# Performance work log

Hardware: AMD Instinct MI355X
Metric: run time of the kernel (lower is better)

Reference implementation:

```python
import jax, jax.numpy as jnp
import numpy as np

INPUT_DIM = 256
DEPTH = 8
HIDDEN = 64
NUM_INNER = 2 ** DEPTH - 1   # 255
NUM_LEAVES = 2 ** DEPTH      # 256
BATCH = 8192


def _xavier(key, shape, fan_in, fan_out):
    bound = jnp.sqrt(6.0 / (fan_in + fan_out)).astype(jnp.float32)
    return jax.random.uniform(key, shape, jnp.float32, -bound, bound)


def setup_inputs() -> dict:
    key = jax.random.key(0)
    k = jax.random.split(key, 5)
    x = jax.random.normal(k[0], (BATCH, INPUT_DIM), jnp.float32)
    # Batched per-node MLP params (one slice per inner node)
    w1 = _xavier(k[1], (NUM_INNER, HIDDEN, INPUT_DIM), INPUT_DIM, HIDDEN)
    b1 = jnp.zeros((NUM_INNER, HIDDEN), jnp.float32)
    w2 = _xavier(k[2], (NUM_INNER, HIDDEN), HIDDEN, 1)
    b2 = jnp.zeros((NUM_INNER,), jnp.float32)
    leaf = _xavier(k[3], (NUM_LEAVES, 1), NUM_LEAVES, 1)
    return {"x": x, "w1": w1, "b1": b1, "w2": w2, "b2": b2, "leaf": leaf}


def reference(x, w1, b1, w2, b2, leaf):
    B = x.shape[0]
    # Fused per-node MLPs: hidden [B, N, H]
    h = jax.nn.relu(jnp.einsum("bi,nhi->bnh", x, w1) + b1)
    logits = jnp.einsum("bnh,nh->bn", h, w2) + b2        # [B, N]
    node_outputs = jax.nn.sigmoid(logits)                 # p, in BFS node order

    # Tree traversal: level-by-level interleave. Child of node j at a level
    # are 2j (left, weight 1-p) and 2j+1 (right, weight p) at the next level.
    reach_levels = []
    cur = jnp.ones((B, 1), x.dtype)
    for level in range(DEPTH):
        reach_levels.append(cur)
        lo = (1 << level) - 1
        p_lvl = node_outputs[:, lo : lo + (1 << level)]   # [B, 2^level]
        cur = jnp.stack([cur * (1.0 - p_lvl), cur * p_lvl], axis=-1).reshape(B, -1)
    node_reach = jnp.concatenate(reach_levels, axis=1)    # [B, NUM_INNER], BFS order
    path_probs = cur                                      # [B, NUM_LEAVES]

    h_out = (path_probs @ leaf)[:, 0]                     # [B]
    return h_out, path_probs, node_outputs, node_reach
```

## Files before the change

kernel.cpp:

```cpp
#include <hip/hip_runtime.h>
#include <cstdint>

#define BATCH   8192
#define KDIM    256
#define HID     64
#define NODES   255
#define NPG     16

typedef unsigned short u16;
typedef short bf16x8 __attribute__((ext_vector_type(8)));
typedef float f32x16 __attribute__((ext_vector_type(16)));


__device__ __forceinline__ unsigned int f2bf(float f) {
  unsigned int u = __float_as_uint(f);
  return (u + 0x7FFFu + ((u >> 16) & 1u)) >> 16;
}

__device__ __forceinline__ void gld_lds16(const void* g, void* l) {
  typedef __attribute__((address_space(1))) void* gp_t;
  typedef __attribute__((address_space(3))) void* lp_t;
  gp_t gp = reinterpret_cast<gp_t>(reinterpret_cast<uintptr_t>(g));
  lp_t lp = reinterpret_cast<lp_t>(static_cast<unsigned int>(reinterpret_cast<uintptr_t>(l)));
  __builtin_amdgcn_global_load_lds(gp, lp, 16, 0, 0);
}


#define NW4  1044480
#define NPRM 16320

__global__ __launch_bounds__(256) void cvt_kernel(
    const float* __restrict__ x, const float* __restrict__ w1,
    const float* __restrict__ b1, const float* __restrict__ w2,
    u16* __restrict__ xpack, u16* __restrict__ w1b,
    float* __restrict__ b1p, float* __restrict__ w2p) {
  const int tid = threadIdx.x;
  const int blk = blockIdx.x;

  if (blk < 256) {
    __shared__ u16 sT[32 * 268];
    const float* xs = x + (size_t)blk * 32 * KDIM;
#pragma unroll
    for (int j = 0; j < 8; ++j) {
      int idx = j * 256 + tid;
      float4 v = ((const float4*)xs)[idx];
      int row = idx >> 6, f4 = idx & 63;
      uint2 o;
      o.x = f2bf(v.x) | (f2bf(v.y) << 16);
      o.y = f2bf(v.z) | (f2bf(v.w) << 16);
      *(uint2*)&sT[row * 268 + f4 * 4] = o;
    }
    __syncthreads();
#pragma unroll
    for (int j = 0; j < 4; ++j) {
      int d = j * 256 + tid;
      int ks = d >> 6, hl = (d >> 5) & 1, l31 = d & 31;
      const u16* s8 = &sT[l31 * 268 + ks * 16 + hl * 8];
      uint2 lo = *(const uint2*)s8;
      uint2 hi = *(const uint2*)(s8 + 4);
      uint4 o = {lo.x, lo.y, hi.x, hi.y};
      ((uint4*)xpack)[(size_t)blk * 1024 + d] = o;
    }
  } else if (blk < 4336) {
    int j = (blk - 256) * 256 + tid;
    float4 v = ((const float4*)w1)[j];
    uint2 o;
    o.x = f2bf(v.x) | (f2bf(v.y) << 16);
    o.y = f2bf(v.z) | (f2bf(v.w) << 16);
    ((uint2*)w1b)[j] = o;
  } else {
    int i2 = (blk - 4336) * 256 + tid;
    if (i2 < 2 * NPRM) {
      int a = i2 >= NPRM;
      int j = a ? i2 - NPRM : i2;
      int reg = j & 15, rt = (j >> 4) & 1, hl = (j >> 5) & 1, node = j >> 6;
      int h = rt * 32 + (reg & 3) + 8 * (reg >> 2) + 4 * hl;
      float v = (a ? b1 : w2)[node * 64 + h];
      (a ? b1p : w2p)[j] = v;
    }
  }
}


__global__ __launch_bounds__(256, 2) void fused_mlp_kernel(
    const u16* __restrict__ xpack,
    const u16* __restrict__ w1b,
    const float* __restrict__ b1p,
    const float* __restrict__ w2p,
    const float* __restrict__ b2,
    float* __restrict__ no_t)
{
  __shared__ __align__(16) u16 sW[2][HID * KDIM];
  __shared__ __align__(16) float sW2[NPG * 64];
  __shared__ __align__(16) float sB1[NPG * 64];

  const int tid  = threadIdx.x;
  const int lane = tid & 63;
  const int wv   = tid >> 6;
  const int l31  = lane & 31;
  const int hl   = lane >> 5;
  const int nbase = blockIdx.y * NPG;
  const int ctile0 = blockIdx.x * 8 + wv * 2;

  auto stage = [&](int node, int buf) {
    const u16* base = w1b + (size_t)node * (HID * KDIM);
    char* lb = (char*)(&sW[buf][0]);
#pragma unroll
    for (int j = 0; j < 8; ++j) {
      int s = j * 256 + tid;
      int h = s >> 5;
      int kb = (s & 31) ^ (h & 31);
      gld_lds16(base + h * KDIM + kb * 8, lb + s * 16);
    }
  };

  stage(nbase, 0);
  gld_lds16(w2p + (size_t)nbase * 64 + tid * 4, (char*)sW2 + tid * 16);
  gld_lds16(b1p + (size_t)nbase * 64 + tid * 4, (char*)sB1 + tid * 16);

  bf16x8 xf[2][16];
#pragma unroll
  for (int ct = 0; ct < 2; ++ct) {
    const u16* src = xpack + ((size_t)(ctile0 + ct) * 16) * 512 + lane * 8;
#pragma unroll
    for (int ks = 0; ks < 16; ++ks)
      xf[ct][ks] = *(const bf16x8*)(src + ks * 512);
  }

  __syncthreads();
  int buf = 0;

  for (int i = 0; i < NPG; ++i) {
    const int node = nbase + i;
    if (i + 1 < NPG) stage(node + 1, buf ^ 1);

    f32x16 acc[2][2];
#pragma unroll
    for (int rt = 0; rt < 2; ++rt)
#pragma unroll
      for (int ct = 0; ct < 2; ++ct) acc[rt][ct] = (f32x16){0};

    const char* sw = (const char*)&sW[buf][0];
#pragma unroll
    for (int ks = 0; ks < 16; ++ks) {
      int t = (ks * 2 + hl) ^ l31;
      bf16x8 a0 = *(const bf16x8*)(sw + (unsigned int)(l31 * 32 + t) * 16u);
      bf16x8 a1 = *(const bf16x8*)(sw + (unsigned int)((32 + l31) * 32 + t) * 16u);
#pragma unroll
      for (int ct = 0; ct < 2; ++ct) {
        acc[0][ct] = __builtin_amdgcn_mfma_f32_32x32x16_bf16(a0, xf[ct][ks], acc[0][ct], 0, 0, 0);
        acc[1][ct] = __builtin_amdgcn_mfma_f32_32x32x16_bf16(a1, xf[ct][ks], acc[1][ct], 0, 0, 0);
      }
    }

    float p0 = 0.f, p1 = 0.f;
#pragma unroll
    for (int rt = 0; rt < 2; ++rt)
#pragma unroll
      for (int qd = 0; qd < 4; ++qd) {
        int o = i * 64 + hl * 32 + rt * 16 + qd * 4;
        float4 wq = *(const float4*)&sW2[o];
        float4 bq = *(const float4*)&sB1[o];
#pragma unroll
        for (int e = 0; e < 4; ++e) {
          float w = (&wq.x)[e];
          float bb = (&bq.x)[e];
          p0 += fmaxf(acc[rt][0][qd * 4 + e] + bb, 0.f) * w;
          p1 += fmaxf(acc[rt][1][qd * 4 + e] + bb, 0.f) * w;
        }
      }
    p0 += __shfl_xor(p0, 32);
    p1 += __shfl_xor(p1, 32);

    if (node < NODES) {
      float logit = (hl ? p1 : p0) + b2[node];
      float sig = 1.0f / (1.0f + expf(-logit));
      no_t[(size_t)node * BATCH + blockIdx.x * 256 + wv * 64 + lane] = sig;
    }

    __syncthreads();
    buf ^= 1;
  }
}


__global__ __launch_bounds__(256) void tree_kernel(
    const float* __restrict__ no_t,
    const float* __restrict__ leaf,
    float* __restrict__ out)
{
  __shared__ float p[16][257];

  const int tid = threadIdx.x;
  const int bbase = blockIdx.x * 16;
  const int wave = tid >> 6;
  const int lane = tid & 63;

  for (int i = tid; i < NODES * 16; i += 256) {
    int n = i >> 4, r = i & 15;
    p[r][n] = no_t[(size_t)n * BATCH + bbase + r];
  }
  __syncthreads();

  float4 lw = ((const float4*)leaf)[lane];

  float* h_out  = out;
  float* pp_out = out + 8192;
  float* no_out = out + 8192 + 8192 * 256;
  float* nr_out = out + 8192 + 8192 * 256 + 8192 * (size_t)NODES;

  for (int j = 0; j < 4; ++j) {
    const int r = wave * 4 + j;
    const int b = bbase + r;
    const float* pr = p[r];
    float* nr_b = nr_out + (size_t)b * NODES;

    float rc = 1.f;
#pragma unroll
    for (int L = 0; L < 6; ++L) {
      if (lane < (1 << L)) nr_b[(1 << L) - 1 + lane] = rc;
      float par = __shfl(rc, lane >> 1);
      float pv = pr[(1 << L) - 1 + (lane >> 1)];
      rc = par * ((lane & 1) ? pv : (1.f - pv));
    }
    nr_b[63 + lane] = rc;
    float p6 = pr[63 + lane];
    float r7a = rc * (1.f - p6), r7b = rc * p6;
    nr_b[127 + 2 * lane]     = r7a;
    nr_b[127 + 2 * lane + 1] = r7b;
    float p7a = pr[127 + 2 * lane], p7b = pr[127 + 2 * lane + 1];
    float4 pp;
    pp.x = r7a * (1.f - p7a);
    pp.y = r7a * p7a;
    pp.z = r7b * (1.f - p7b);
    pp.w = r7b * p7b;
    ((float4*)(pp_out + (size_t)b * 256))[lane] = pp;

    float* no_b = no_out + (size_t)b * NODES;
#pragma unroll
    for (int k = 0; k < 4; ++k) {
      int n = lane + 64 * k;
      if (n < NODES) no_b[n] = pr[n];
    }

    float hacc = pp.x * lw.x + pp.y * lw.y + pp.z * lw.z + pp.w * lw.w;
    hacc += __shfl_xor(hacc, 1);
    hacc += __shfl_xor(hacc, 2);
    hacc += __shfl_xor(hacc, 4);
    hacc += __shfl_xor(hacc, 8);
    hacc += __shfl_xor(hacc, 16);
    hacc += __shfl_xor(hacc, 32);
    if (lane == 0) h_out[b] = hacc;
  }
}


extern "C" void kernel_launch(void* const* d_in, const int* in_sizes, int n_in,
                              void* d_out, int out_size, void* d_ws, size_t ws_size,
                              hipStream_t stream) {
  const float* x    = (const float*)d_in[0];
  const float* w1   = (const float*)d_in[1];
  const float* b1   = (const float*)d_in[2];
  const float* w2   = (const float*)d_in[3];
  const float* b2   = (const float*)d_in[4];
  const float* leaf = (const float*)d_in[5];
  float* out = (float*)d_out;

  char* ws = (char*)d_ws;
  u16*   xpack = (u16*)ws;
  u16*   w1b   = (u16*)(ws + (size_t)4194304);
  float* w2p   = (float*)(ws + (size_t)12582912);
  float* b1p   = (float*)(ws + (size_t)12648192);
  float* no_t  = (float*)(ws + (size_t)12713472);

  cvt_kernel<<<4464, 256, 0, stream>>>(x, w1, b1, w2, xpack, w1b, b1p, w2p);

  dim3 g(32, 16);
  fused_mlp_kernel<<<g, 256, 0, stream>>>(xpack, w1b, b1p, w2p, b2, no_t);

  tree_kernel<<<BATCH / 16, 256, 0, stream>>>(no_t, leaf, out);
}
```

Baseline: 159.8 us.

## Pre-pack W1 into MFMA fragment order and split row tiles across waves

The conversion kernel now transposes each node's W1 into the exact MFMA A-fragment order, so the fused kernel stages weights with plain contiguous copies and reads them without XOR swizzle arithmetic. Each wave now handles one 32-row tile for two column tiles instead of both row tiles. Partial logits are combined across wave pairs through a small LDS buffer, and the grid is doubled so each block covers 128 batch rows. This trades fewer LDS loads per wave and more blocks for an extra cross-wave reduction, a barrier placed before the sigmoid, and doubled weight staging traffic per batch row.

```diff
diff --git a/kernel.cpp b/kernel.cpp
--- a/kernel.cpp
+++ b/kernel.cpp
@@ -8,12 +8,13 @@
 #define NPG     16
 
 typedef unsigned short u16;
+typedef unsigned int u32;
 typedef short bf16x8 __attribute__((ext_vector_type(8)));
 typedef float f32x16 __attribute__((ext_vector_type(16)));
 
 
-__device__ __forceinline__ unsigned int f2bf(float f) {
-  unsigned int u = __float_as_uint(f);
+__device__ __forceinline__ u32 f2bf(float f) {
+  u32 u = __float_as_uint(f);
   return (u + 0x7FFFu + ((u >> 16) & 1u)) >> 16;
 }
 
@@ -21,18 +22,17 @@
   typedef __attribute__((address_space(1))) void* gp_t;
   typedef __attribute__((address_space(3))) void* lp_t;
   gp_t gp = reinterpret_cast<gp_t>(reinterpret_cast<uintptr_t>(g));
-  lp_t lp = reinterpret_cast<lp_t>(static_cast<unsigned int>(reinterpret_cast<uintptr_t>(l)));
+  lp_t lp = reinterpret_cast<lp_t>(static_cast<u32>(reinterpret_cast<uintptr_t>(l)));
   __builtin_amdgcn_global_load_lds(gp, lp, 16, 0, 0);
 }
 
 
-#define NW4  1044480
 #define NPRM 16320
 
 __global__ __launch_bounds__(256) void cvt_kernel(
     const float* __restrict__ x, const float* __restrict__ w1,
     const float* __restrict__ b1, const float* __restrict__ w2,
-    u16* __restrict__ xpack, u16* __restrict__ w1b,
+    u16* __restrict__ xpack, u16* __restrict__ w1pk,
     float* __restrict__ b1p, float* __restrict__ w2p) {
   const int tid = threadIdx.x;
   const int blk = blockIdx.x;
@@ -45,10 +45,8 @@
       int idx = j * 256 + tid;
       float4 v = ((const float4*)xs)[idx];
       int row = idx >> 6, f4 = idx & 63;
-      uint2 o;
-      o.x = f2bf(v.x) | (f2bf(v.y) << 16);
-      o.y = f2bf(v.z) | (f2bf(v.w) << 16);
-      *(uint2*)&sT[row * 268 + f4 * 4] = o;
+      *(u32*)&sT[row * 268 + f4 * 4]     = f2bf(v.x) | (f2bf(v.y) << 16);
+      *(u32*)&sT[row * 268 + f4 * 4 + 2] = f2bf(v.z) | (f2bf(v.w) << 16);
     }
     __syncthreads();
 #pragma unroll
@@ -56,20 +54,39 @@
       int d = j * 256 + tid;
       int ks = d >> 6, hl = (d >> 5) & 1, l31 = d & 31;
       const u16* s8 = &sT[l31 * 268 + ks * 16 + hl * 8];
+      u32 a = *(const u32*)s8, b = *(const u32*)(s8 + 2);
+      u32 c = *(const u32*)(s8 + 4), e = *(const u32*)(s8 + 6);
+      uint4 o = {a, b, c, e};
+      ((uint4*)xpack)[(size_t)blk * 1024 + d] = o;
+    }
+  } else if (blk < 511) {
+    __shared__ u16 sT[64 * 260];
+    const int node = blk - 256;
+    const float* src = w1 + (size_t)node * (HID * KDIM);
+#pragma unroll
+    for (int r = 0; r < 16; ++r) {
+      int idx = r * 256 + tid;
+      float4 v = ((const float4*)src)[idx];
+      int h = idx >> 6, f4 = idx & 63;
+      uint2 o;
+      o.x = f2bf(v.x) | (f2bf(v.y) << 16);
+      o.y = f2bf(v.z) | (f2bf(v.w) << 16);
+      *(uint2*)&sT[h * 260 + f4 * 4] = o;
+    }
+    __syncthreads();
+    u16* dst = w1pk + (size_t)node * (HID * KDIM);
+#pragma unroll
+    for (int r = 0; r < 8; ++r) {
+      int g = r * 256 + tid;
+      int kb = g >> 6, h = g & 63;
+      const u16* s8 = &sT[h * 260 + kb * 8];
       uint2 lo = *(const uint2*)s8;
       uint2 hi = *(const uint2*)(s8 + 4);
       uint4 o = {lo.x, lo.y, hi.x, hi.y};
-      ((uint4*)xpack)[(size_t)blk * 1024 + d] = o;
-    }
-  } else if (blk < 4336) {
-    int j = (blk - 256) * 256 + tid;
-    float4 v = ((const float4*)w1)[j];
-    uint2 o;
-    o.x = f2bf(v.x) | (f2bf(v.y) << 16);
-    o.y = f2bf(v.z) | (f2bf(v.w) << 16);
-    ((uint2*)w1b)[j] = o;
+      ((uint4*)dst)[g] = o;
+    }
   } else {
-    int i2 = (blk - 4336) * 256 + tid;
+    int i2 = (blk - 511) * 256 + tid;
     if (i2 < 2 * NPRM) {
       int a = i2 >= NPRM;
       int j = a ? i2 - NPRM : i2;
@@ -82,9 +99,11 @@
 }
 
 
-__global__ __launch_bounds__(256, 2) void fused_mlp_kernel(
+__global__ void __attribute__((amdgpu_flat_work_group_size(256, 256),
+                               amdgpu_waves_per_eu(2, 2)))
+fused_mlp_kernel(
     const u16* __restrict__ xpack,
-    const u16* __restrict__ w1b,
+    const u16* __restrict__ w1pk,
     const float* __restrict__ b1p,
     const float* __restrict__ w2p,
     const float* __restrict__ b2,
@@ -93,24 +112,24 @@
   __shared__ __align__(16) u16 sW[2][HID * KDIM];
   __shared__ __align__(16) float sW2[NPG * 64];
   __shared__ __align__(16) float sB1[NPG * 64];
+  __shared__ float sP[2][4][64];
 
   const int tid  = threadIdx.x;
   const int lane = tid & 63;
   const int wv   = tid >> 6;
   const int l31  = lane & 31;
   const int hl   = lane >> 5;
+  const int rt   = wv & 1;
+  const int ch   = wv >> 1;
   const int nbase = blockIdx.y * NPG;
-  const int ctile0 = blockIdx.x * 8 + wv * 2;
 
   auto stage = [&](int node, int buf) {
-    const u16* base = w1b + (size_t)node * (HID * KDIM);
+    const u16* base = w1pk + (size_t)node * (HID * KDIM);
     char* lb = (char*)(&sW[buf][0]);
 #pragma unroll
     for (int j = 0; j < 8; ++j) {
       int s = j * 256 + tid;
-      int h = s >> 5;
-      int kb = (s & 31) ^ (h & 31);
-      gld_lds16(base + h * KDIM + kb * 8, lb + s * 16);
+      gld_lds16(base + s * 8, lb + s * 16);
     }
   };
 
@@ -118,6 +137,7 @@
   gld_lds16(w2p + (size_t)nbase * 64 + tid * 4, (char*)sW2 + tid * 16);
   gld_lds16(b1p + (size_t)nbase * 64 + tid * 4, (char*)sB1 + tid * 16);
 
+  const int ctile0 = blockIdx.x * 4 + ch * 2;
   bf16x8 xf[2][16];
 #pragma unroll
   for (int ct = 0; ct < 2; ++ct) {
@@ -127,59 +147,56 @@
       xf[ct][ks] = *(const bf16x8*)(src + ks * 512);
   }
 
+  const u32 abase = (u32)(hl * 64 + rt * 32 + l31) * 16u;
+
   __syncthreads();
-  int buf = 0;
+  int buf = 0, par = 0;
 
   for (int i = 0; i < NPG; ++i) {
     const int node = nbase + i;
     if (i + 1 < NPG) stage(node + 1, buf ^ 1);
 
-    f32x16 acc[2][2];
-#pragma unroll
-    for (int rt = 0; rt < 2; ++rt)
-#pragma unroll
-      for (int ct = 0; ct < 2; ++ct) acc[rt][ct] = (f32x16){0};
-
-    const char* sw = (const char*)&sW[buf][0];
+    f32x16 acc0 = (f32x16){0}, acc1 = (f32x16){0};
+    const char* sw = (const char*)&sW[buf][0] + abase;
 #pragma unroll
     for (int ks = 0; ks < 16; ++ks) {
-      int t = (ks * 2 + hl) ^ l31;
-      bf16x8 a0 = *(const bf16x8*)(sw + (unsigned int)(l31 * 32 + t) * 16u);
-      bf16x8 a1 = *(const bf16x8*)(sw + (unsigned int)((32 + l31) * 32 + t) * 16u);
-#pragma unroll
-      for (int ct = 0; ct < 2; ++ct) {
-        acc[0][ct] = __builtin_amdgcn_mfma_f32_32x32x16_bf16(a0, xf[ct][ks], acc[0][ct], 0, 0, 0);
-        acc[1][ct] = __builtin_amdgcn_mfma_f32_32x32x16_bf16(a1, xf[ct][ks], acc[1][ct], 0, 0, 0);
+      bf16x8 a = *(const bf16x8*)(sw + ks * 2048);
+      acc0 = __builtin_amdgcn_mfma_f32_32x32x16_bf16(a, xf[0][ks], acc0, 0, 0, 0);
+      acc1 = __builtin_amdgcn_mfma_f32_32x32x16_bf16(a, xf[1][ks], acc1, 0, 0, 0);
+    }
+
+    float p0 = 0.f, p1 = 0.f;
+#pragma unroll
+    for (int qd = 0; qd < 4; ++qd) {
+      int o = i * 64 + hl * 32 + rt * 16 + qd * 4;
+      float4 wq = *(const float4*)&sW2[o];
+      float4 bq = *(const float4*)&sB1[o];
+#pragma unroll
+      for (int e = 0; e < 4; ++e) {
+        float w = (&wq.x)[e];
+        float bb = (&bq.x)[e];
+        p0 += fmaxf(acc0[qd * 4 + e] + bb, 0.f) * w;
+        p1 += fmaxf(acc1[qd * 4 + e] + bb, 0.f) * w;
       }
     }
-
-    float p0 = 0.f, p1 = 0.f;
-#pragma unroll
-    for (int rt = 0; rt < 2; ++rt)
-#pragma unroll
-      for (int qd = 0; qd < 4; ++qd) {
-        int o = i * 64 + hl * 32 + rt * 16 + qd * 4;
-        float4 wq = *(const float4*)&sW2[o];
-        float4 bq = *(const float4*)&sB1[o];
-#pragma unroll
-        for (int e = 0; e < 4; ++e) {
-          float w = (&wq.x)[e];
-          float bb = (&bq.x)[e];
-          p0 += fmaxf(acc[rt][0][qd * 4 + e] + bb, 0.f) * w;
-          p1 += fmaxf(acc[rt][1][qd * 4 + e] + bb, 0.f) * w;
-        }
-      }
     p0 += __shfl_xor(p0, 32);
     p1 += __shfl_xor(p1, 32);
-
-    if (node < NODES) {
-      float logit = (hl ? p1 : p0) + b2[node];
+    if (hl == 0) {
+      sP[par][wv][l31]      = p0;
+      sP[par][wv][32 + l31] = p1;
+    }
+
+    __syncthreads();
+
+    if (tid < 128 && node < NODES) {
+      int chh = tid >> 6, c = tid & 63;
+      float logit = sP[par][chh * 2][c] + sP[par][chh * 2 + 1][c] + b2[node];
       float sig = 1.0f / (1.0f + expf(-logit));
-      no_t[(size_t)node * BATCH + blockIdx.x * 256 + wv * 64 + lane] = sig;
-    }
-
-    __syncthreads();
+      no_t[(size_t)node * BATCH + blockIdx.x * 128 + tid] = sig;
+    }
+
     buf ^= 1;
+    par ^= 1;
   }
 }
 
@@ -268,15 +285,15 @@
 
   char* ws = (char*)d_ws;
   u16*   xpack = (u16*)ws;
-  u16*   w1b   = (u16*)(ws + (size_t)4194304);
+  u16*   w1pk  = (u16*)(ws + (size_t)4194304);
   float* w2p   = (float*)(ws + (size_t)12582912);
   float* b1p   = (float*)(ws + (size_t)12648192);
   float* no_t  = (float*)(ws + (size_t)12713472);
 
-  cvt_kernel<<<4464, 256, 0, stream>>>(x, w1, b1, w2, xpack, w1b, b1p, w2p);
-
-  dim3 g(32, 16);
-  fused_mlp_kernel<<<g, 256, 0, stream>>>(xpack, w1b, b1p, w2p, b2, no_t);
+  cvt_kernel<<<639, 256, 0, stream>>>(x, w1, b1, w2, xpack, w1pk, b1p, w2p);
+
+  dim3 g(64, 16);
+  fused_mlp_kernel<<<g, 256, 0, stream>>>(xpack, w1pk, b1p, w2p, b2, no_t);
 
   tree_kernel<<<BATCH / 16, 256, 0, stream>>>(no_t, leaf, out);
 }
```

After: 159.8 us. No clear change (-0.0%).
